# Kernel tuning notes

Hardware: AMD Instinct MI355X
Metric: run time of the kernel (lower is better)

Reference implementation:

```python
import jax, jax.numpy as jnp
import numpy as np

B, T, IN, H, L = 16, 256, 256, 1024, 4

def setup_inputs() -> dict:
    key = jax.random.key(0)
    ks = jax.random.split(key, 5)
    return {
        "x": jax.random.normal(ks[0], (B, T, IN), jnp.float32),
        # gate axis order: 0=forget, 1=input-perc(sigmoid), 2=input-pot(tanh), 3=output
        "Wh": jax.random.normal(ks[1], (L, 4, H, H), jnp.float32) * 0.1,
        "Wx0": jax.random.normal(ks[2], (4, IN, H), jnp.float32) * 0.1,
        "Wx": jax.random.normal(ks[3], (L - 1, 4, H, H), jnp.float32) * 0.1,
        "b": jax.random.normal(ks[4], (L, 4, H), jnp.float32) * 0.1,
    }

def _run_layer(inp, wh, wx, bias):
    # inp: [B, T, D]; wh: [4, H, H]; wx: [4, D, H]; bias: [4, H]
    # Precompute all input projections for every timestep (time-major for scan).
    pre = jnp.einsum('btd,gdh->tbgh', inp, wx) + bias  # [T, B, 4, H]
    Bn = inp.shape[0]
    Hn = wh.shape[-1]

    def step(carry, px):
        h, c = carry  # short_term, long_term
        g = px + jnp.einsum('bh,gho->bgo', h, wh)  # [B, 4, H]
        f = jax.nn.sigmoid(g[:, 0])       # forget factor
        perc = jax.nn.sigmoid(g[:, 1])    # input gate (percent)
        pot = jnp.tanh(g[:, 2])           # input gate (potential)
        o = jax.nn.sigmoid(g[:, 3])       # output gate (uses OLD short_term)
        c_new = f * c + perc * pot
        h_new = jnp.tanh(c_new) * o
        return (h_new, c_new), h_new

    init = (jnp.zeros((Bn, Hn), inp.dtype), jnp.zeros((Bn, Hn), inp.dtype))
    (h, _), hs = jax.lax.scan(step, init, pre)
    return h, jnp.moveaxis(hs, 0, 1)  # final hidden [B,H], all hiddens [B,T,H]

def reference(x, Wh, Wx0, Wx, b):
    h, seq = _run_layer(x, Wh[0], Wx0, b[0])
    for i in range(1, Wh.shape[0]):
        h, seq = _run_layer(seq, Wh[i], Wx[i - 1], b[i])
    return h  # original returns (final_hidden, None); None dropped
```

## Files before the change

kernel.cpp:

```cpp
#include <hip/hip_runtime.h>


typedef float f32x4 __attribute__((ext_vector_type(4)));
typedef short bf16x8 __attribute__((ext_vector_type(8)));

__device__ __forceinline__ unsigned short f2bf_rn(float x) {
    unsigned int u = __float_as_uint(x);
    u += 0x7FFFu + ((u >> 16) & 1u);
    return (unsigned short)(u >> 16);
}
__device__ __forceinline__ float bf2f(unsigned short s) {
    return __uint_as_float(((unsigned int)s) << 16);
}
__device__ __forceinline__ float sigmoidf_(float x) { return 1.0f / (1.0f + __expf(-x)); }
__device__ __forceinline__ float tanhf_(float x) {
    float e = __expf(2.0f * x);
    return 1.0f - 2.0f / (e + 1.0f);
}

#define MFMA16(a, b, c) __builtin_amdgcn_mfma_f32_16x16x32_bf16((a), (b), (c), 0, 0, 0)

__global__ __launch_bounds__(256)
void pre_gemm(const float* __restrict__ A, const float* __restrict__ W,
              const float* __restrict__ bias, float* __restrict__ out, int K)
{
    __shared__ float As[16][132];
    __shared__ float Bs[16][132];

    const int tid = threadIdx.x;
    const int m0 = blockIdx.y << 7;
    const int n0 = blockIdx.x << 7;
    const int g  = n0 >> 10;
    const int jb = n0 & 1023;
    const float* Wg = W + (size_t)g * K * 1024 + jb;

    const int tx = tid & 15;
    const int ty = tid >> 4;
    const int alk = tid & 15;
    const int alm = tid >> 4;
    const int bln = tid & 127;
    const int blkk = tid >> 7;

    float acc[8][8];
#pragma unroll
    for (int i = 0; i < 8; ++i)
#pragma unroll
        for (int j = 0; j < 8; ++j) acc[i][j] = 0.f;

    for (int k0 = 0; k0 < K; k0 += 16) {
        __syncthreads();
#pragma unroll
        for (int r = 0; r < 8; ++r) {
            int m = alm + (r << 4);
            As[alk][m] = A[(size_t)(m0 + m) * K + (k0 + alk)];
        }
#pragma unroll
        for (int r = 0; r < 8; ++r) {
            int kk = blkk + (r << 1);
            Bs[kk][bln] = Wg[(size_t)(k0 + kk) * 1024 + bln];
        }
        __syncthreads();
#pragma unroll
        for (int k = 0; k < 16; ++k) {
            float a[8], bb[8];
            *(f32x4*)&a[0]  = *(const f32x4*)&As[k][ty << 2];
            *(f32x4*)&a[4]  = *(const f32x4*)&As[k][64 + (ty << 2)];
            *(f32x4*)&bb[0] = *(const f32x4*)&Bs[k][tx << 2];
            *(f32x4*)&bb[4] = *(const f32x4*)&Bs[k][64 + (tx << 2)];
#pragma unroll
            for (int i = 0; i < 8; ++i)
#pragma unroll
                for (int j = 0; j < 8; ++j)
                    acc[i][j] = fmaf(a[i], bb[j], acc[i][j]);
        }
    }

    float bj[8];
#pragma unroll
    for (int j = 0; j < 8; ++j) {
        int nloc = (j < 4) ? ((tx << 2) + j) : (64 + (tx << 2) + (j - 4));
        bj[j] = bias[n0 + nloc];
    }
#pragma unroll
    for (int i = 0; i < 8; ++i) {
        int mloc = (i < 4) ? ((ty << 2) + i) : (64 + (ty << 2) + (i - 4));
        int m = m0 + mloc;
        int bidx = m >> 8;
        int tt   = m & 255;
        float* orow = out + ((size_t)((tt << 4) + bidx) << 12) + n0;
#pragma unroll
        for (int j = 0; j < 8; ++j) {
            int nloc = (j < 4) ? ((tx << 2) + j) : (64 + (tx << 2) + (j - 4));
            orow[nloc] = acc[i][j] + bj[j];
        }
    }
}

__global__ __launch_bounds__(256)
void lstm_scan(const float* __restrict__ pre,
               const float* __restrict__ Wh,
               float* __restrict__ seq_out,
               unsigned short* __restrict__ hhi,
               unsigned short* __restrict__ hlo,
               int* __restrict__ ctr_l1,
               float* __restrict__ final_out,
               int is_last)
{
    const int wg   = blockIdx.x;
    const int tid  = threadIdx.x;
    const int wv   = tid >> 6;
    const int lane = tid & 63;
    const int bc   = lane & 15;
    const int quad = lane >> 4;

    __shared__ float red[4][64][4];
    __shared__ float gsh[16][17];

    const int g   = bc >> 2;
    const int col = (wg << 2) + (bc & 3);
    bf16x8 Whi[8], Wmi[8], Wlo[8];
#pragma unroll
    for (int ck = 0; ck < 8; ++ck) {
#pragma unroll
        for (int j = 0; j < 8; ++j) {
            int k = (wv << 8) + (ck << 5) + (quad << 3) + j;
            float w = Wh[((size_t)g << 20) + ((size_t)k << 10) + col];
            unsigned short hi = f2bf_rn(w);
            float r1 = w - bf2f(hi);
            unsigned short mi = f2bf_rn(r1);
            float r2 = r1 - bf2f(mi);
            unsigned short lo = f2bf_rn(r2);
            Whi[ck][j] = (short)hi;
            Wmi[ck][j] = (short)mi;
            Wlo[ck][j] = (short)lo;
        }
    }

    float creg = 0.f;
    int dead = 0;

    for (int t = 0; t < 256; ++t) {
        float pr[4];
        if (wv == 0) {
            const float* pp = pre + ((size_t)t << 16) + ((size_t)(bc >> 2) << 10)
                              + (wg << 2) + (bc & 3);
#pragma unroll
            for (int r = 0; r < 4; ++r)
                pr[r] = pp[(size_t)((quad << 2) + r) << 12];
        }

        if (t > 0 && wv == 0 && !dead) {
            const int* lb = ctr_l1 + (((t - 1) << 4) << 5);
            bool done = (lane >= 16);
            const int gi5 = (lane & 15) << 5;
            int guard = 0;
            for (;;) {
                if (!done)
                    done = __hip_atomic_load(lb + gi5, __ATOMIC_RELAXED,
                                             __HIP_MEMORY_SCOPE_AGENT) >= 16;
                if (__all(done)) break;
                __builtin_amdgcn_s_sleep(1);
                if (++guard > (1 << 15)) { dead = 1; break; }
            }
        }
        __syncthreads();
        asm volatile("" ::: "memory");

        f32x4 a00 = {0.f, 0.f, 0.f, 0.f};
        f32x4 a01 = a00, a10 = a00, a11 = a00;
        if (t > 0) {
            const size_t pb = ((size_t)(t - 1) << 14) + ((size_t)bc << 10) + (wv << 8);
            const unsigned short* ph = hhi + pb;
            const unsigned short* pl = hlo + pb;
            bf16x8 ahi[8], alo[8];
#pragma unroll
            for (int ck = 0; ck < 8; ++ck) {
                ahi[ck] = *(const bf16x8*)(ph + (ck << 5) + (quad << 3));
                alo[ck] = *(const bf16x8*)(pl + (ck << 5) + (quad << 3));
            }
#pragma unroll
            for (int ck = 0; ck < 8; ++ck) {
                if (ck & 1) {
                    a10 = MFMA16(ahi[ck], Whi[ck], a10);
                    a11 = MFMA16(ahi[ck], Wmi[ck], a11);
                    a10 = MFMA16(ahi[ck], Wlo[ck], a10);
                    a11 = MFMA16(alo[ck], Whi[ck], a11);
                    a10 = MFMA16(alo[ck], Wmi[ck], a10);
                } else {
                    a00 = MFMA16(ahi[ck], Whi[ck], a00);
                    a01 = MFMA16(ahi[ck], Wmi[ck], a01);
                    a00 = MFMA16(ahi[ck], Wlo[ck], a00);
                    a01 = MFMA16(alo[ck], Whi[ck], a01);
                    a00 = MFMA16(alo[ck], Wmi[ck], a00);
                }
            }
        }
        f32x4 acc = (a00 + a01) + (a10 + a11);
        *(f32x4*)&red[wv][lane][0] = acc;
        __syncthreads();

        if (wv == 0) {
            f32x4 s0 = *(const f32x4*)&red[0][lane][0];
            f32x4 s1 = *(const f32x4*)&red[1][lane][0];
            f32x4 s2 = *(const f32x4*)&red[2][lane][0];
            f32x4 s3 = *(const f32x4*)&red[3][lane][0];
            f32x4 s = (s0 + s1) + (s2 + s3);
#pragma unroll
            for (int r = 0; r < 4; ++r)
                gsh[(quad << 2) + r][bc] = s[r] + pr[r];

            const int b2 = lane >> 2, jl2 = lane & 3;
            float fg = sigmoidf_(gsh[b2][jl2]);
            float ig = sigmoidf_(gsh[b2][4 + jl2]);
            float pg = tanhf_(gsh[b2][8 + jl2]);
            float og = sigmoidf_(gsh[b2][12 + jl2]);
            creg = fg * creg + ig * pg;
            float h = tanhf_(creg) * og;

            const int j = (wg << 2) + jl2;
            unsigned short hh = f2bf_rn(h);
            unsigned short hl = f2bf_rn(h - bf2f(hh));
            size_t pidx = ((size_t)t << 14) + ((size_t)b2 << 10) + j;
            __hip_atomic_store(&hhi[pidx], hh, __ATOMIC_RELAXED, __HIP_MEMORY_SCOPE_AGENT);
            __hip_atomic_store(&hlo[pidx], hl, __ATOMIC_RELAXED, __HIP_MEMORY_SCOPE_AGENT);
            if (is_last && t == 255) final_out[((size_t)b2 << 10) + j] = h;

            __builtin_amdgcn_s_waitcnt(0);
            if (lane == 0)
                __hip_atomic_fetch_add(&ctr_l1[((t << 4) + (wg >> 4)) << 5], 1,
                                       __ATOMIC_RELAXED,
                                       __HIP_MEMORY_SCOPE_AGENT);

            if (!is_last)
                seq_out[((size_t)((b2 << 8) + t) << 10) + j] = h;
        }
    }
}

__global__ __launch_bounds__(512)
void lstm_pair(const float* __restrict__ preA,
               const float* __restrict__ WhA,
               const float* __restrict__ WhB,
               const float* __restrict__ WxB,
               const float* __restrict__ biasB,
               float* __restrict__ seq_out,
               unsigned short* __restrict__ hAhi, unsigned short* __restrict__ hAlo,
               unsigned short* __restrict__ hBhi, unsigned short* __restrict__ hBlo,
               int* __restrict__ ctrA,
               int* __restrict__ ctrB,
               float* __restrict__ final_out,
               int is_last)
{
    const int wg   = blockIdx.x;
    const int tid  = threadIdx.x;
    const int wv   = tid >> 6;
    const int lane = tid & 63;
    const int bc   = lane & 15;
    const int quad = lane >> 4;

    __shared__ float red[3][8][64][4];
    __shared__ float gsh[2][16][17];
    __shared__ float ring[2][16][17];

    const int g   = bc >> 2;
    const int col = (wg << 2) + (bc & 3);

    bf16x8 WAh[4], WAm[4], WAl[4];
    bf16x8 WBh[4], WBm[4], WBl[4];
    bf16x8 WXh[4], WXm[4], WXl[4];
#pragma unroll
    for (int ck = 0; ck < 4; ++ck) {
#pragma unroll
        for (int j = 0; j < 8; ++j) {
            const int k = (wv << 7) + (ck << 5) + (quad << 3) + j;
            const size_t widx = ((size_t)g << 20) + ((size_t)k << 10) + col;
            {
                float w = WhA[widx];
                unsigned short hi = f2bf_rn(w); float r1 = w - bf2f(hi);
                unsigned short mi = f2bf_rn(r1); float r2 = r1 - bf2f(mi);
                WAh[ck][j] = (short)hi; WAm[ck][j] = (short)mi;
                WAl[ck][j] = (short)f2bf_rn(r2);
            }
            {
                float w = WhB[widx];
                unsigned short hi = f2bf_rn(w); float r1 = w - bf2f(hi);
                unsigned short mi = f2bf_rn(r1); float r2 = r1 - bf2f(mi);
                WBh[ck][j] = (short)hi; WBm[ck][j] = (short)mi;
                WBl[ck][j] = (short)f2bf_rn(r2);
            }
            {
                float w = WxB[widx];
                unsigned short hi = f2bf_rn(w); float r1 = w - bf2f(hi);
                unsigned short mi = f2bf_rn(r1); float r2 = r1 - bf2f(mi);
                WXh[ck][j] = (short)hi; WXm[ck][j] = (short)mi;
                WXl[ck][j] = (short)f2bf_rn(r2);
            }
        }
    }
    const float biasv = biasB[((size_t)g << 10) + col];

    float creg = 0.f;
    int dead = 0;

    for (int s = 0; s < 258; ++s) {
        float pr[4];
        if (wv == 0 && s < 256) {
            const float* pp = preA + ((size_t)s << 16) + ((size_t)g << 10) + col;
#pragma unroll
            for (int r = 0; r < 4; ++r)
                pr[r] = pp[(size_t)((quad << 2) + r) << 12];
        }

        if (s > 0 && wv == 0 && !dead) {
            bool done;
            const int gi = lane & 15;
            const int* wp;
            if (lane < 16)      { done = (s > 256); wp = ctrA + (((s - 1) << 4) + gi) * 32; }
            else if (lane < 32) { done = (s < 3);   wp = ctrB + (((s - 1) << 4) + gi) * 32; }
            else                { done = true;      wp = ctrA; }
            int guard = 0;
            for (;;) {
                if (!done)
                    done = __hip_atomic_load(wp, __ATOMIC_RELAXED,
                                             __HIP_MEMORY_SCOPE_AGENT) >= 16;
                if (__all(done)) break;
                __builtin_amdgcn_s_sleep(1);
                if (++guard > (1 << 14)) { dead = 1; break; }
            }
        }
        __syncthreads();
        asm volatile("" ::: "memory");

        f32x4 aA0 = {0.f, 0.f, 0.f, 0.f}, aA1 = aA0;
        f32x4 aP0 = aA0, aP1 = aA0;
        f32x4 aB0 = aA0, aB1 = aA0;

        if (s >= 1 && s <= 256) {
            const size_t pb = ((size_t)(s - 1) << 14) + ((size_t)bc << 10) + (wv << 7);
            const unsigned short* ph = hAhi + pb;
            const unsigned short* pl = hAlo + pb;
#pragma unroll
            for (int ck = 0; ck < 4; ++ck) {
                bf16x8 ah = *(const bf16x8*)(ph + (ck << 5) + (quad << 3));
                bf16x8 al = *(const bf16x8*)(pl + (ck << 5) + (quad << 3));
                if (ck & 1) {
                    aA1 = MFMA16(ah, WAh[ck], aA1);
                    aA1 = MFMA16(ah, WAm[ck], aA1);
                    aA1 = MFMA16(ah, WAl[ck], aA1);
                    aA1 = MFMA16(al, WAh[ck], aA1);
                    aA1 = MFMA16(al, WAm[ck], aA1);
                    aP1 = MFMA16(ah, WXh[ck], aP1);
                    aP1 = MFMA16(ah, WXm[ck], aP1);
                    aP1 = MFMA16(ah, WXl[ck], aP1);
                    aP1 = MFMA16(al, WXh[ck], aP1);
                    aP1 = MFMA16(al, WXm[ck], aP1);
                } else {
                    aA0 = MFMA16(ah, WAh[ck], aA0);
                    aA0 = MFMA16(ah, WAm[ck], aA0);
                    aA0 = MFMA16(ah, WAl[ck], aA0);
                    aA0 = MFMA16(al, WAh[ck], aA0);
                    aA0 = MFMA16(al, WAm[ck], aA0);
                    aP0 = MFMA16(ah, WXh[ck], aP0);
                    aP0 = MFMA16(ah, WXm[ck], aP0);
                    aP0 = MFMA16(ah, WXl[ck], aP0);
                    aP0 = MFMA16(al, WXh[ck], aP0);
                    aP0 = MFMA16(al, WXm[ck], aP0);
                }
            }
        }
        if (s >= 3) {
            const size_t pb = ((size_t)(s - 3) << 14) + ((size_t)bc << 10) + (wv << 7);
            const unsigned short* ph = hBhi + pb;
            const unsigned short* pl = hBlo + pb;
#pragma unroll
            for (int ck = 0; ck < 4; ++ck) {
                bf16x8 bh = *(const bf16x8*)(ph + (ck << 5) + (quad << 3));
                bf16x8 bl = *(const bf16x8*)(pl + (ck << 5) + (quad << 3));
                if (ck & 1) {
                    aB1 = MFMA16(bh, WBh[ck], aB1);
                    aB1 = MFMA16(bh, WBm[ck], aB1);
                    aB1 = MFMA16(bh, WBl[ck], aB1);
                    aB1 = MFMA16(bl, WBh[ck], aB1);
                    aB1 = MFMA16(bl, WBm[ck], aB1);
                } else {
                    aB0 = MFMA16(bh, WBh[ck], aB0);
                    aB0 = MFMA16(bh, WBm[ck], aB0);
                    aB0 = MFMA16(bh, WBl[ck], aB0);
                    aB0 = MFMA16(bl, WBh[ck], aB0);
                    aB0 = MFMA16(bl, WBm[ck], aB0);
                }
            }
        }

        *(f32x4*)&red[0][wv][lane][0] = aA0 + aA1;
        *(f32x4*)&red[1][wv][lane][0] = aP0 + aP1;
        *(f32x4*)&red[2][wv][lane][0] = aB0 + aB1;
        __syncthreads();

        if (wv == 0) {
            if (s <= 255) {
                f32x4 sm = {0.f, 0.f, 0.f, 0.f};
#pragma unroll
                for (int w = 0; w < 8; ++w)
                    sm += *(const f32x4*)&red[0][w][lane][0];
#pragma unroll
                for (int r = 0; r < 4; ++r)
                    gsh[0][(quad << 2) + r][bc] = sm[r] + pr[r];

                const int b2 = lane >> 2, jl2 = lane & 3;
                float fg = sigmoidf_(gsh[0][b2][jl2]);
                float ig = sigmoidf_(gsh[0][b2][4 + jl2]);
                float pg = tanhf_(gsh[0][b2][8 + jl2]);
                float og = sigmoidf_(gsh[0][b2][12 + jl2]);
                creg = fg * creg + ig * pg;
                float h = tanhf_(creg) * og;
                const int j = (wg << 2) + jl2;
                unsigned short hh = f2bf_rn(h);
                unsigned short hl = f2bf_rn(h - bf2f(hh));
                size_t pidx = ((size_t)s << 14) + ((size_t)b2 << 10) + j;
                __hip_atomic_store(&hAhi[pidx], hh, __ATOMIC_RELAXED, __HIP_MEMORY_SCOPE_AGENT);
                __hip_atomic_store(&hAlo[pidx], hl, __ATOMIC_RELAXED, __HIP_MEMORY_SCOPE_AGENT);
                __builtin_amdgcn_s_waitcnt(0);
                if (lane == 0)
                    __hip_atomic_fetch_add(&ctrA[((s << 4) + (wg >> 4)) << 5], 1,
                                           __ATOMIC_RELAXED,
                                           __HIP_MEMORY_SCOPE_AGENT);
            }
        } else if (wv == 1) {
            if (s >= 2) {
                const int t1 = s - 2;
                f32x4 sm = {0.f, 0.f, 0.f, 0.f};
#pragma unroll
                for (int w = 0; w < 8; ++w)
                    sm += *(const f32x4*)&red[2][w][lane][0];
#pragma unroll
                for (int r = 0; r < 4; ++r)
                    gsh[1][(quad << 2) + r][bc] =
                        sm[r] + ring[t1 & 1][(quad << 2) + r][bc];

                const int b2 = lane >> 2, jl2 = lane & 3;
                float fg = sigmoidf_(gsh[1][b2][jl2]);
                float ig = sigmoidf_(gsh[1][b2][4 + jl2]);
                float pg = tanhf_(gsh[1][b2][8 + jl2]);
                float og = sigmoidf_(gsh[1][b2][12 + jl2]);
                creg = fg * creg + ig * pg;
                float h = tanhf_(creg) * og;
                const int j = (wg << 2) + jl2;
                unsigned short hh = f2bf_rn(h);
                unsigned short hl = f2bf_rn(h - bf2f(hh));
                size_t pidx = ((size_t)t1 << 14) + ((size_t)b2 << 10) + j;
                __hip_atomic_store(&hBhi[pidx], hh, __ATOMIC_RELAXED, __HIP_MEMORY_SCOPE_AGENT);
                __hip_atomic_store(&hBlo[pidx], hl, __ATOMIC_RELAXED, __HIP_MEMORY_SCOPE_AGENT);
                __builtin_amdgcn_s_waitcnt(0);
                if (lane == 0)
                    __hip_atomic_fetch_add(&ctrB[((s << 4) + (wg >> 4)) << 5], 1,
                                           __ATOMIC_RELAXED,
                                           __HIP_MEMORY_SCOPE_AGENT);
                if (!is_last)
                    seq_out[((size_t)((b2 << 8) + t1) << 10) + j] = h;
                if (is_last && t1 == 255)
                    final_out[((size_t)b2 << 10) + j] = h;
            }
        } else if (wv == 2) {
            if (s >= 1 && s <= 256) {
                f32x4 qm = {0.f, 0.f, 0.f, 0.f};
#pragma unroll
                for (int w = 0; w < 8; ++w)
                    qm += *(const f32x4*)&red[1][w][lane][0];
#pragma unroll
                for (int r = 0; r < 4; ++r)
                    ring[(s - 1) & 1][(quad << 2) + r][bc] = qm[r] + biasv;
            }
        }
    }
}

extern "C" void kernel_launch(void* const* d_in, const int* in_sizes, int n_in,
                              void* d_out, int out_size, void* d_ws, size_t ws_size,
                              hipStream_t stream)
{
    (void)in_sizes; (void)n_in; (void)out_size; (void)ws_size;

    const float* x    = (const float*)d_in[0];
    const float* Wh   = (const float*)d_in[1];
    const float* Wx0  = (const float*)d_in[2];
    const float* Wx   = (const float*)d_in[3];
    const float* bias = (const float*)d_in[4];

    float* pre  = (float*)d_ws;
    float* seqA = pre + 16777216;
    float* reg2 = seqA + 4194304;
    unsigned short* hAhi = (unsigned short*)(reg2 + 4194304);
    unsigned short* hAlo = hAhi + 4194304;
    int* ctr = (int*)(hAlo + 4194304);
    const size_t PAIR_PL = 258 * 16 * 32;
    const size_t FB_PL   = 256 * 16 * 32;

    float* fout = (float*)d_out;
    const dim3 blk(256);
    const dim3 blkP(512);
    const dim3 ggrid(32, 32);
    const size_t WLAYER = (size_t)4 * 1024 * 1024;

    int nb = 0;
    if (hipOccupancyMaxActiveBlocksPerMultiprocessor(&nb, lstm_pair, 512, 0)
        != hipSuccess) nb = 0;

    hipMemsetAsync(ctr, 0, 4 * PAIR_PL * sizeof(int), stream);

    if (nb >= 1) {
        unsigned short* hBhi = (unsigned short*)reg2;
        unsigned short* hBlo = hBhi + 4194304;

        pre_gemm<<<ggrid, blk, 0, stream>>>(x, Wx0, bias, pre, 256);
        for (int p01 = 0; p01 < 2; ++p01) {
            const float* p   = pre;
            const float* whA = Wh + (size_t)(2 * p01) * WLAYER;
            const float* whB = Wh + (size_t)(2 * p01 + 1) * WLAYER;
            const float* wxB = Wx + (size_t)(2 * p01) * WLAYER;
            const float* bB  = bias + (size_t)(2 * p01 + 1) * 4096;
            float* so = seqA;
            int* cA = ctr + (size_t)(2 * p01) * PAIR_PL;
            int* cB = cA + PAIR_PL;
            int last = (p01 == 1);
            void* args[] = { (void*)&p, (void*)&whA, (void*)&whB, (void*)&wxB,
                             (void*)&bB, (void*)&so, (void*)&hAhi, (void*)&hAlo,
                             (void*)&hBhi, (void*)&hBlo, (void*)&cA, (void*)&cB,
                             (void*)&fout, (void*)&last };
            hipLaunchCooperativeKernel((void*)lstm_pair, dim3(256), blkP, args, 0, stream);
            if (p01 == 0)
                pre_gemm<<<ggrid, blk, 0, stream>>>(seqA, Wx + WLAYER,
                                                    bias + 2 * 4096, pre, 1024);
        }
    } else {
        float* seqB = reg2;
        unsigned short* hhi = hAhi;
        unsigned short* hlo = hAlo;
        for (int l = 0; l < 4; ++l) {
            const float* inp = (l == 0) ? x : ((l & 1) ? seqA : seqB);
            float* outp      = (l & 1) ? seqB : seqA;
            const float* wx  = (l == 0) ? Wx0 : (Wx + (size_t)(l - 1) * WLAYER);
            int K            = (l == 0) ? 256 : 1024;

            pre_gemm<<<ggrid, blk, 0, stream>>>(inp, wx, bias + (size_t)l * 4096, pre, K);

            const float* p = pre;
            const float* wh = Wh + (size_t)l * WLAYER;
            float* so = outp;
            int* pl1 = ctr + (size_t)l * FB_PL;
            int last = (l == 3);
            void* args[] = { (void*)&p, (void*)&wh, (void*)&so, (void*)&hhi,
                             (void*)&hlo, (void*)&pl1, (void*)&fout, (void*)&last };
            hipLaunchCooperativeKernel((void*)lstm_scan, dim3(256), blk, args, 0, stream);
        }
    }
}
```

Measured before the change: 6.879 ms.

## Restructure fused layer-pair step to put layer-A recurrence on the critical path first

Each step of the fused two-layer kernel now computes only layer A's recurrent MFMAs, reduces them, and publishes h_A before doing the layer-B input projection and layer-B recurrence in a second phase with its own barrier. The projection results go into a triple-buffered shared ring, and layer B lags by four steps instead of two, which gives more slack between the layers. The aim is to shorten the latency between consecutive h_A publications so cross-workgroup waits on layer A resolve sooner. The cost is an extra __syncthreads per step, more shared memory, two extra loop iterations, and a longer pipeline fill and drain.

```diff
diff --git a/kernel.cpp b/kernel.cpp
--- a/kernel.cpp
+++ b/kernel.cpp
@@ -258,7 +258,9 @@
     const int bc   = lane & 15;
     const int quad = lane >> 4;
 
-    __shared__ float red[3][8][64][4];
+    __shared__ float redA[8][64][4];
+    __shared__ float redP[3][8][64][4];
+    __shared__ float redB[2][8][64][4];
     __shared__ float gsh[2][16][17];
     __shared__ float ring[2][16][17];
 
@@ -299,10 +301,11 @@
     }
     const float biasv = biasB[((size_t)g << 10) + col];
 
-    float creg = 0.f;
+    float cregA = 0.f;
+    float cregB = 0.f;
     int dead = 0;
 
-    for (int s = 0; s < 258; ++s) {
+    for (int s = 0; s < 260; ++s) {
         float pr[4];
         if (wv == 0 && s < 256) {
             const float* pp = preA + ((size_t)s << 16) + ((size_t)g << 10) + col;
@@ -311,12 +314,12 @@
                 pr[r] = pp[(size_t)((quad << 2) + r) << 12];
         }
 
-        if (s > 0 && wv == 0 && !dead) {
+        if (s >= 1 && wv == 0 && !dead) {
             bool done;
             const int gi = lane & 15;
             const int* wp;
             if (lane < 16)      { done = (s > 256); wp = ctrA + (((s - 1) << 4) + gi) * 32; }
-            else if (lane < 32) { done = (s < 3);   wp = ctrB + (((s - 1) << 4) + gi) * 32; }
+            else if (lane < 32) { done = (s < 5);   wp = ctrB + (((s - 5) << 4) + gi) * 32; }
             else                { done = true;      wp = ctrA; }
             int guard = 0;
             for (;;) {
@@ -325,17 +328,14 @@
                                              __HIP_MEMORY_SCOPE_AGENT) >= 16;
                 if (__all(done)) break;
                 __builtin_amdgcn_s_sleep(1);
-                if (++guard > (1 << 14)) { dead = 1; break; }
+                if (++guard > (1 << 15)) { dead = 1; break; }
             }
         }
         __syncthreads();
         asm volatile("" ::: "memory");
 
-        f32x4 aA0 = {0.f, 0.f, 0.f, 0.f}, aA1 = aA0;
-        f32x4 aP0 = aA0, aP1 = aA0;
-        f32x4 aB0 = aA0, aB1 = aA0;
-
-        if (s >= 1 && s <= 256) {
+        f32x4 a0 = {0.f, 0.f, 0.f, 0.f}, a1 = a0;
+        if (s >= 1 && s <= 255) {
             const size_t pb = ((size_t)(s - 1) << 14) + ((size_t)bc << 10) + (wv << 7);
             const unsigned short* ph = hAhi + pb;
             const unsigned short* pl = hAlo + pb;
@@ -344,57 +344,21 @@
                 bf16x8 ah = *(const bf16x8*)(ph + (ck << 5) + (quad << 3));
                 bf16x8 al = *(const bf16x8*)(pl + (ck << 5) + (quad << 3));
                 if (ck & 1) {
-                    aA1 = MFMA16(ah, WAh[ck], aA1);
-                    aA1 = MFMA16(ah, WAm[ck], aA1);
-                    aA1 = MFMA16(ah, WAl[ck], aA1);
-                    aA1 = MFMA16(al, WAh[ck], aA1);
-                    aA1 = MFMA16(al, WAm[ck], aA1);
-                    aP1 = MFMA16(ah, WXh[ck], aP1);
-                    aP1 = MFMA16(ah, WXm[ck], aP1);
-                    aP1 = MFMA16(ah, WXl[ck], aP1);
-                    aP1 = MFMA16(al, WXh[ck], aP1);
-                    aP1 = MFMA16(al, WXm[ck], aP1);
+                    a1 = MFMA16(ah, WAh[ck], a1);
+                    a1 = MFMA16(ah, WAm[ck], a1);
+                    a1 = MFMA16(ah, WAl[ck], a1);
+                    a1 = MFMA16(al, WAh[ck], a1);
+                    a1 = MFMA16(al, WAm[ck], a1);
                 } else {
-                    aA0 = MFMA16(ah, WAh[ck], aA0);
-                    aA0 = MFMA16(ah, WAm[ck], aA0);
-                    aA0 = MFMA16(ah, WAl[ck], aA0);
-                    aA0 = MFMA16(al, WAh[ck], aA0);
-                    aA0 = MFMA16(al, WAm[ck], aA0);
-                    aP0 = MFMA16(ah, WXh[ck], aP0);
-                    aP0 = MFMA16(ah, WXm[ck], aP0);
-                    aP0 = MFMA16(ah, WXl[ck], aP0);
-                    aP0 = MFMA16(al, WXh[ck], aP0);
-                    aP0 = MFMA16(al, WXm[ck], aP0);
+                    a0 = MFMA16(ah, WAh[ck], a0);
+                    a0 = MFMA16(ah, WAm[ck], a0);
+                    a0 = MFMA16(ah, WAl[ck], a0);
+                    a0 = MFMA16(al, WAh[ck], a0);
+                    a0 = MFMA16(al, WAm[ck], a0);
                 }
             }
         }
-        if (s >= 3) {
-            const size_t pb = ((size_t)(s - 3) << 14) + ((size_t)bc << 10) + (wv << 7);
-            const unsigned short* ph = hBhi + pb;
-            const unsigned short* pl = hBlo + pb;
-#pragma unroll
-            for (int ck = 0; ck < 4; ++ck) {
-                bf16x8 bh = *(const bf16x8*)(ph + (ck << 5) + (quad << 3));
-                bf16x8 bl = *(const bf16x8*)(pl + (ck << 5) + (quad << 3));
-                if (ck & 1) {
-                    aB1 = MFMA16(bh, WBh[ck], aB1);
-                    aB1 = MFMA16(bh, WBm[ck], aB1);
-                    aB1 = MFMA16(bh, WBl[ck], aB1);
-                    aB1 = MFMA16(bl, WBh[ck], aB1);
-                    aB1 = MFMA16(bl, WBm[ck], aB1);
-                } else {
-                    aB0 = MFMA16(bh, WBh[ck], aB0);
-                    aB0 = MFMA16(bh, WBm[ck], aB0);
-                    aB0 = MFMA16(bh, WBl[ck], aB0);
-                    aB0 = MFMA16(bl, WBh[ck], aB0);
-                    aB0 = MFMA16(bl, WBm[ck], aB0);
-                }
-            }
-        }
-
-        *(f32x4*)&red[0][wv][lane][0] = aA0 + aA1;
-        *(f32x4*)&red[1][wv][lane][0] = aP0 + aP1;
-        *(f32x4*)&red[2][wv][lane][0] = aB0 + aB1;
+        *(f32x4*)&redA[wv][lane][0] = a0 + a1;
         __syncthreads();
 
         if (wv == 0) {
@@ -402,7 +366,7 @@
                 f32x4 sm = {0.f, 0.f, 0.f, 0.f};
 #pragma unroll
                 for (int w = 0; w < 8; ++w)
-                    sm += *(const f32x4*)&red[0][w][lane][0];
+                    sm += *(const f32x4*)&redA[w][lane][0];
 #pragma unroll
                 for (int r = 0; r < 4; ++r)
                     gsh[0][(quad << 2) + r][bc] = sm[r] + pr[r];
@@ -412,8 +376,8 @@
                 float ig = sigmoidf_(gsh[0][b2][4 + jl2]);
                 float pg = tanhf_(gsh[0][b2][8 + jl2]);
                 float og = sigmoidf_(gsh[0][b2][12 + jl2]);
-                creg = fg * creg + ig * pg;
-                float h = tanhf_(creg) * og;
+                cregA = fg * cregA + ig * pg;
+                float h = tanhf_(cregA) * og;
                 const int j = (wg << 2) + jl2;
                 unsigned short hh = f2bf_rn(h);
                 unsigned short hl = f2bf_rn(h - bf2f(hh));
@@ -426,51 +390,108 @@
                                            __ATOMIC_RELAXED,
                                            __HIP_MEMORY_SCOPE_AGENT);
             }
-        } else if (wv == 1) {
-            if (s >= 2) {
-                const int t1 = s - 2;
-                f32x4 sm = {0.f, 0.f, 0.f, 0.f};
+        } else if (wv == 2) {
+            if (s >= 3 && s <= 258) {
+                const int u = s - 3;
+                f32x4 qm = {0.f, 0.f, 0.f, 0.f};
 #pragma unroll
                 for (int w = 0; w < 8; ++w)
-                    sm += *(const f32x4*)&red[2][w][lane][0];
+                    qm += *(const f32x4*)&redP[u % 3][w][lane][0];
 #pragma unroll
                 for (int r = 0; r < 4; ++r)
-                    gsh[1][(quad << 2) + r][bc] =
-                        sm[r] + ring[t1 & 1][(quad << 2) + r][bc];
-
-                const int b2 = lane >> 2, jl2 = lane & 3;
-                float fg = sigmoidf_(gsh[1][b2][jl2]);
-                float ig = sigmoidf_(gsh[1][b2][4 + jl2]);
-                float pg = tanhf_(gsh[1][b2][8 + jl2]);
-                float og = sigmoidf_(gsh[1][b2][12 + jl2]);
-                creg = fg * creg + ig * pg;
-                float h = tanhf_(creg) * og;
-                const int j = (wg << 2) + jl2;
-                unsigned short hh = f2bf_rn(h);
-                unsigned short hl = f2bf_rn(h - bf2f(hh));
-                size_t pidx = ((size_t)t1 << 14) + ((size_t)b2 << 10) + j;
-                __hip_atomic_store(&hBhi[pidx], hh, __ATOMIC_RELAXED, __HIP_MEMORY_SCOPE_AGENT);
-                __hip_atomic_store(&hBlo[pidx], hl, __ATOMIC_RELAXED, __HIP_MEMORY_SCOPE_AGENT);
-                __builtin_amdgcn_s_waitcnt(0);
-                if (lane == 0)
-                    __hip_atomic_fetch_add(&ctrB[((s << 4) + (wg >> 4)) << 5], 1,
-                                           __ATOMIC_RELAXED,
-                                           __HIP_MEMORY_SCOPE_AGENT);
-                if (!is_last)
-                    seq_out[((size_t)((b2 << 8) + t1) << 10) + j] = h;
-                if (is_last && t1 == 255)
-                    final_out[((size_t)b2 << 10) + j] = h;
-            }
-        } else if (wv == 2) {
-            if (s >= 1 && s <= 256) {
-                f32x4 qm = {0.f, 0.f, 0.f, 0.f};
-#pragma unroll
-                for (int w = 0; w < 8; ++w)
-                    qm += *(const f32x4*)&red[1][w][lane][0];
-#pragma unroll
-                for (int r = 0; r < 4; ++r)
-                    ring[(s - 1) & 1][(quad << 2) + r][bc] = qm[r] + biasv;
-            }
+                    ring[u & 1][(quad << 2) + r][bc] = qm[r] + biasv;
+            }
+        }
+
+        if (s >= 1 && s <= 256) {
+            const size_t pb = ((size_t)(s - 1) << 14) + ((size_t)bc << 10) + (wv << 7);
+            const unsigned short* ph = hAhi + pb;
+            const unsigned short* pl = hAlo + pb;
+            f32x4 p0 = {0.f, 0.f, 0.f, 0.f}, p1 = p0;
+#pragma unroll
+            for (int ck = 0; ck < 4; ++ck) {
+                bf16x8 ah = *(const bf16x8*)(ph + (ck << 5) + (quad << 3));
+                bf16x8 al = *(const bf16x8*)(pl + (ck << 5) + (quad << 3));
+                if (ck & 1) {
+                    p1 = MFMA16(ah, WXh[ck], p1);
+                    p1 = MFMA16(ah, WXm[ck], p1);
+                    p1 = MFMA16(ah, WXl[ck], p1);
+                    p1 = MFMA16(al, WXh[ck], p1);
+                    p1 = MFMA16(al, WXm[ck], p1);
+                } else {
+                    p0 = MFMA16(ah, WXh[ck], p0);
+                    p0 = MFMA16(ah, WXm[ck], p0);
+                    p0 = MFMA16(ah, WXl[ck], p0);
+                    p0 = MFMA16(al, WXh[ck], p0);
+                    p0 = MFMA16(al, WXm[ck], p0);
+                }
+            }
+            *(f32x4*)&redP[(s - 1) % 3][wv][lane][0] = p0 + p1;
+        }
+
+        if (s >= 4 && s <= 259) {
+            const int u = s - 4;
+            f32x4 b0 = {0.f, 0.f, 0.f, 0.f}, b1 = b0;
+            if (u >= 1) {
+                const size_t pb = ((size_t)(u - 1) << 14) + ((size_t)bc << 10) + (wv << 7);
+                const unsigned short* ph = hBhi + pb;
+                const unsigned short* pl = hBlo + pb;
+#pragma unroll
+                for (int ck = 0; ck < 4; ++ck) {
+                    bf16x8 bh = *(const bf16x8*)(ph + (ck << 5) + (quad << 3));
+                    bf16x8 bl = *(const bf16x8*)(pl + (ck << 5) + (quad << 3));
+                    if (ck & 1) {
+                        b1 = MFMA16(bh, WBh[ck], b1);
+                        b1 = MFMA16(bh, WBm[ck], b1);
+                        b1 = MFMA16(bh, WBl[ck], b1);
+                        b1 = MFMA16(bl, WBh[ck], b1);
+                        b1 = MFMA16(bl, WBm[ck], b1);
+                    } else {
+                        b0 = MFMA16(bh, WBh[ck], b0);
+                        b0 = MFMA16(bh, WBm[ck], b0);
+                        b0 = MFMA16(bh, WBl[ck], b0);
+                        b0 = MFMA16(bl, WBh[ck], b0);
+                        b0 = MFMA16(bl, WBm[ck], b0);
+                    }
+                }
+            }
+            *(f32x4*)&redB[u & 1][wv][lane][0] = b0 + b1;
+        }
+        __syncthreads();
+
+        if (wv == 1 && s >= 4 && s <= 259) {
+            const int u = s - 4;
+            f32x4 sm = {0.f, 0.f, 0.f, 0.f};
+#pragma unroll
+            for (int w = 0; w < 8; ++w)
+                sm += *(const f32x4*)&redB[u & 1][w][lane][0];
+#pragma unroll
+            for (int r = 0; r < 4; ++r)
+                gsh[1][(quad << 2) + r][bc] =
+                    sm[r] + ring[u & 1][(quad << 2) + r][bc];
+
+            const int b2 = lane >> 2, jl2 = lane & 3;
+            float fg = sigmoidf_(gsh[1][b2][jl2]);
+            float ig = sigmoidf_(gsh[1][b2][4 + jl2]);
+            float pg = tanhf_(gsh[1][b2][8 + jl2]);
+            float og = sigmoidf_(gsh[1][b2][12 + jl2]);
+            cregB = fg * cregB + ig * pg;
+            float h = tanhf_(cregB) * og;
+            const int j = (wg << 2) + jl2;
+            unsigned short hh = f2bf_rn(h);
+            unsigned short hl = f2bf_rn(h - bf2f(hh));
+            size_t pidx = ((size_t)u << 14) + ((size_t)b2 << 10) + j;
+            __hip_atomic_store(&hBhi[pidx], hh, __ATOMIC_RELAXED, __HIP_MEMORY_SCOPE_AGENT);
+            __hip_atomic_store(&hBlo[pidx], hl, __ATOMIC_RELAXED, __HIP_MEMORY_SCOPE_AGENT);
+            __builtin_amdgcn_s_waitcnt(0);
+            if (lane == 0)
+                __hip_atomic_fetch_add(&ctrB[((u << 4) + (wg >> 4)) << 5], 1,
+                                       __ATOMIC_RELAXED,
+                                       __HIP_MEMORY_SCOPE_AGENT);
+            if (!is_last)
+                seq_out[(((size_t)(b2 << 8) + u) << 10) + j] = h;
+            if (is_last && u == 255)
+                final_out[((size_t)b2 << 10) + j] = h;
         }
     }
 }
@@ -493,8 +514,7 @@
     unsigned short* hAhi = (unsigned short*)(reg2 + 4194304);
     unsigned short* hAlo = hAhi + 4194304;
     int* ctr = (int*)(hAlo + 4194304);
-    const size_t PAIR_PL = 258 * 16 * 32;
-    const size_t FB_PL   = 256 * 16 * 32;
+    const size_t PL = 256 * 16 * 32;
 
     float* fout = (float*)d_out;
     const dim3 blk(256);
@@ -506,7 +526,7 @@
     if (hipOccupancyMaxActiveBlocksPerMultiprocessor(&nb, lstm_pair, 512, 0)
         != hipSuccess) nb = 0;
 
-    hipMemsetAsync(ctr, 0, 4 * PAIR_PL * sizeof(int), stream);
+    hipMemsetAsync(ctr, 0, 4 * PL * sizeof(int), stream);
 
     if (nb >= 1) {
         unsigned short* hBhi = (unsigned short*)reg2;
@@ -520,8 +540,8 @@
             const float* wxB = Wx + (size_t)(2 * p01) * WLAYER;
             const float* bB  = bias + (size_t)(2 * p01 + 1) * 4096;
             float* so = seqA;
-            int* cA = ctr + (size_t)(2 * p01) * PAIR_PL;
-            int* cB = cA + PAIR_PL;
+            int* cA = ctr + (size_t)(2 * p01) * PL;
+            int* cB = cA + PL;
             int last = (p01 == 1);
             void* args[] = { (void*)&p, (void*)&whA, (void*)&whB, (void*)&wxB,
                              (void*)&bB, (void*)&so, (void*)&hAhi, (void*)&hAlo,
@@ -547,7 +567,7 @@
             const float* p = pre;
             const float* wh = Wh + (size_t)l * WLAYER;
             float* so = outp;
-            int* pl1 = ctr + (size_t)l * FB_PL;
+            int* pl1 = ctr + (size_t)l * PL;
             int last = (l == 3);
             void* args[] = { (void*)&p, (void*)&wh, (void*)&so, (void*)&hhi,
                              (void*)&hlo, (void*)&pl1, (void*)&fout, (void*)&last };
```

After: 6.745 ms. Within noise of the previous version (-2.0%).
